# Optimization experiments

Hardware: AMD Instinct MI355X
Metric: run time of the kernel (lower is better)

The kernel has to match this reference:

```python
import jax, jax.numpy as jnp
import numpy as np

NU, NI, D, K, L, E, B = 500000, 200000, 64, 4, 3, 2000000, 131072

def setup_inputs() -> dict:
    key = jax.random.key(0)
    ks = jax.random.split(key, 7)
    return {
        'user_emb': 0.1 * jax.random.normal(ks[0], (NU, D), dtype=jnp.float32),
        'item_emb': 0.1 * jax.random.normal(ks[1], (NI, D), dtype=jnp.float32),
        'factor_weight': jax.random.normal(ks[2], (K, K), dtype=jnp.float32),
        'edge_users': jax.random.randint(ks[3], (E,), 0, NU),
        'edge_items': jax.random.randint(ks[4], (E,), 0, NI),
        'users': jax.random.randint(ks[5], (B,), 0, NU),
        'items': jax.random.randint(ks[6], (B,), 0, NI),
    }

def reference(user_emb, item_emb, factor_weight, edge_users, edge_items, users, items):
    N = NU + NI
    X = jnp.concatenate([user_emb, item_emb], axis=0)  # [N, D]
    src = edge_users                     # user node ids
    dst = edge_items + NU                # item node ids (offset)
    # symmetric degree normalization 1/sqrt(d_u * d_i) over the bipartite graph
    deg = jnp.zeros((N,), jnp.float32).at[src].add(1.0).at[dst].add(1.0)
    inv_sqrt = jnp.where(deg > 0, jax.lax.rsqrt(jnp.maximum(deg, 1.0)), 0.0)
    w = (inv_sqrt[src] * inv_sqrt[dst])[:, None]  # [E, 1]

    def propagate(x):
        # messages in both directions (A is symmetric)
        out = jnp.zeros_like(x)
        out = out.at[dst].add(x[src] * w)
        out = out.at[src].add(x[dst] * w)
        return out

    acc = X
    x = X
    for _ in range(L):
        x = propagate(x)
        acc = acc + x
    Z = acc / jnp.float32(L + 1)  # LightGCN layer mean

    dk = D // K
    u = Z[users].reshape(B, K, dk)          # user factor embeddings
    i = Z[items + NU].reshape(B, K, dk)     # item factor embeddings
    corr = jnp.einsum('bfd,bgd->bfg', u, i)  # pairwise factor correlations
    scores = jnp.einsum('bfg,fg->b', corr, factor_weight)
    return scores
```

## Files before the change

kernel.cpp:

```cpp
#include <hip/hip_runtime.h>
#include <math.h>

#define NU_ 500000
#define NI_ 200000
#define NN_ 700000
#define D_  64
#define E_  2000000
#define B_  131072
#define TWO_E 4000000

#define SHIFT_ 10
#define NBUCK_ 684
#define BCAP_  12288
#define B1_TILE 16384

typedef _Float16 half4 __attribute__((ext_vector_type(4)));
typedef _Float16 half8 __attribute__((ext_vector_type(8)));

__global__ __launch_bounds__(256) void bucket_hist_kernel(const int* __restrict__ eu,
                                                          const int* __restrict__ ei,
                                                          int* __restrict__ bucketCnt,
                                                          int* __restrict__ rowptr) {
    __shared__ int h[NBUCK_];
    for (int i = threadIdx.x; i < NBUCK_; i += 256) h[i] = 0;
    __syncthreads();
    size_t base = (size_t)blockIdx.x * B1_TILE;
    for (int k = 0; k < 64; ++k) {
        size_t idx = base + (size_t)k * 256 + threadIdx.x;
        if (idx < TWO_E) {
            int e = (int)(idx >> 1);
            int node = (idx & 1) ? (ei[e] + NU_) : eu[e];
            atomicAdd(&h[node >> SHIFT_], 1);
        }
    }
    __syncthreads();
    for (int i = threadIdx.x; i < NBUCK_; i += 256)
        if (h[i]) atomicAdd(&bucketCnt[i], h[i]);
    if (blockIdx.x == 0 && threadIdx.x == 0) rowptr[NN_] = TWO_E;
}

__global__ __launch_bounds__(1024) void scan_block(const int* __restrict__ in, int n,
                                                   int* __restrict__ out,
                                                   int* __restrict__ psum) {
    __shared__ int lds[1024];
    int g = blockIdx.x * 1024 + threadIdx.x;
    int v = (g < n) ? in[g] : 0;
    lds[threadIdx.x] = v;
    __syncthreads();
    for (int off = 1; off < 1024; off <<= 1) {
        int t = (threadIdx.x >= (unsigned)off) ? lds[threadIdx.x - off] : 0;
        __syncthreads();
        lds[threadIdx.x] += t;
        __syncthreads();
    }
    if (g < n) out[g] = lds[threadIdx.x] - v;
    if (threadIdx.x == 1023 && psum) psum[blockIdx.x] = lds[1023];
}

__global__ __launch_bounds__(256) void bucket_scatter_kernel(const int* __restrict__ eu,
                                                             const int* __restrict__ ei,
                                                             int* __restrict__ cursor,
                                                             unsigned long long* __restrict__ pairs) {
    __shared__ int h[NBUCK_];
    __shared__ int basel[NBUCK_];
    for (int i = threadIdx.x; i < NBUCK_; i += 256) h[i] = 0;
    __syncthreads();
    size_t base = (size_t)blockIdx.x * B1_TILE;
    for (int k = 0; k < 64; ++k) {
        size_t idx = base + (size_t)k * 256 + threadIdx.x;
        if (idx < TWO_E) {
            int e = (int)(idx >> 1);
            int node = (idx & 1) ? (ei[e] + NU_) : eu[e];
            atomicAdd(&h[node >> SHIFT_], 1);
        }
    }
    __syncthreads();
    for (int i = threadIdx.x; i < NBUCK_; i += 256) {
        int c = h[i];
        basel[i] = c ? atomicAdd(&cursor[i], c) : 0;
    }
    __syncthreads();
    for (int i = threadIdx.x; i < NBUCK_; i += 256) h[i] = 0;
    __syncthreads();
    for (int k = 0; k < 64; ++k) {
        size_t idx = base + (size_t)k * 256 + threadIdx.x;
        if (idx < TWO_E) {
            int e = (int)(idx >> 1);
            int side = (int)(idx & 1);
            int u = eu[e];
            int v = ei[e] + NU_;
            int node = side ? v : u;
            int nbr  = side ? u : v;
            int bk = node >> SHIFT_;
            int r = atomicAdd(&h[bk], 1);
            pairs[(size_t)basel[bk] + r] =
                ((unsigned long long)(unsigned)node << 32) | (unsigned)nbr;
        }
    }
}

__global__ __launch_bounds__(256) void csr_build_kernel(const unsigned long long* __restrict__ pairs,
                                                        const int* __restrict__ bucketBase,
                                                        int* __restrict__ rowptr,
                                                        int* __restrict__ adj,
                                                        float* __restrict__ inv,
                                                        float* __restrict__ sdeg) {
    __shared__ int cnt[1024];
    __shared__ int sA[1024];
    __shared__ int sB[1024];
    __shared__ int adjl[BCAP_];
    int b  = blockIdx.x;
    int lo = bucketBase[b];
    int hi = (b == NBUCK_ - 1) ? TWO_E : bucketBase[b + 1];
    int sz = hi - lo;
    if (sz > BCAP_) sz = BCAP_;
    int node0 = b << SHIFT_;
    for (int i = threadIdx.x; i < 1024; i += 256) cnt[i] = 0;
    __syncthreads();
    for (int i = threadIdx.x; i < sz; i += 256) {
        int node = (int)(pairs[(size_t)lo + i] >> 32);
        atomicAdd(&cnt[node & 1023], 1);
    }
    __syncthreads();
    for (int i = threadIdx.x; i < 1024; i += 256) sA[i] = cnt[i];
    __syncthreads();
    int* cur = sA; int* nxt = sB;
    for (int off = 1; off < 1024; off <<= 1) {
        for (int i = threadIdx.x; i < 1024; i += 256)
            nxt[i] = cur[i] + (i >= off ? cur[i - off] : 0);
        __syncthreads();
        int* tmp = cur; cur = nxt; nxt = tmp;
    }
    for (int i = threadIdx.x; i < 1024; i += 256) {
        int excl = cur[i] - cnt[i];
        nxt[i] = excl;
        int node = node0 + i;
        if (node < NN_) {
            rowptr[node] = lo + excl;
            int d = cnt[i];
            inv[node]  = d ? (1.0f / sqrtf((float)d)) : 0.0f;
            sdeg[node] = sqrtf((float)d);
        }
    }
    __syncthreads();
    for (int i = threadIdx.x; i < sz; i += 256) {
        unsigned long long p = pairs[(size_t)lo + i];
        int node = (int)(p >> 32);
        int nbr  = (int)(p & 0xffffffffu);
        int r = atomicAdd(&nxt[node & 1023], 1);
        if (r < BCAP_) adjl[r] = nbr;
    }
    __syncthreads();
    for (int i = threadIdx.x; i < sz; i += 256) adj[lo + i] = adjl[i];
}

__global__ __launch_bounds__(256) void conv_kernel(const float* __restrict__ ue,
                                                   const float* __restrict__ ie,
                                                   const float* __restrict__ inv,
                                                   half4* __restrict__ xh) {
    int t = blockIdx.x * 256 + threadIdx.x;
    int b = t >> 4;
    int q = t & 15;
    const float4* src = (b < NU_)
        ? ((const float4*)(ue + (size_t)b * D_) + q)
        : ((const float4*)(ie + (size_t)(b - NU_) * D_) + q);
    float4 a = *src;
    float iv = inv[b];
    half4 h;
    h[0] = (_Float16)(iv * a.x); h[1] = (_Float16)(iv * a.y);
    h[2] = (_Float16)(iv * a.z); h[3] = (_Float16)(iv * a.w);
    xh[(size_t)b * 16 + q] = h;
}

__global__ __launch_bounds__(256) void pull_kernel(const half8* __restrict__ yh,
                                                   const float* __restrict__ inv,
                                                   const int* __restrict__ rowptr,
                                                   const int* __restrict__ adj,
                                                   half8* __restrict__ out) {
    int t = blockIdx.x * 256 + threadIdx.x;
    int v = t >> 6;
    int lane = t & 63;
    int g = lane >> 3;
    int q = lane & 7;
    int beg = rowptr[v];
    int end = rowptr[v + 1];
    float acc[8] = {0.f, 0.f, 0.f, 0.f, 0.f, 0.f, 0.f, 0.f};
    for (int j = beg; j < end; j += 8) {
        int i = j + g;
        int n = adj[i];
        n = (i < end) ? n : NN_;
        half8 a = yh[(size_t)n * 8 + q];
#pragma unroll
        for (int k = 0; k < 8; ++k)
            acc[k] += (float)a[k];
    }
#pragma unroll
    for (int k = 0; k < 8; ++k) {
        acc[k] += __shfl_xor(acc[k], 8);
        acc[k] += __shfl_xor(acc[k], 16);
        acc[k] += __shfl_xor(acc[k], 32);
    }
    if (g == 0) {
        float iv = inv[v];
        float iv2 = iv * iv;
        half8 o;
#pragma unroll
        for (int k = 0; k < 8; ++k) o[k] = (_Float16)(iv2 * acc[k]);
        out[(size_t)v * 8 + q] = o;
    }
}

__device__ __forceinline__ float node_final(int node,
                                            const float* __restrict__ embrow,
                                            const _Float16* __restrict__ y1,
                                            const _Float16* __restrict__ y2,
                                            const float* __restrict__ inv,
                                            const float* __restrict__ sdeg,
                                            const int* __restrict__ rowptr,
                                            const int* __restrict__ adj,
                                            int lane, int g, int q) {
    int beg = rowptr[node];
    int end = rowptr[node + 1];
    float acc[8] = {0.f, 0.f, 0.f, 0.f, 0.f, 0.f, 0.f, 0.f};
    for (int j = beg; j < end; j += 8) {
        int i = j + g;
        int n = adj[i];
        n = (i < end) ? n : NN_;
        half8 a = *(const half8*)(y2 + ((unsigned)n * 64u + (unsigned)q * 8u));
#pragma unroll
        for (int k = 0; k < 8; ++k)
            acc[k] += (float)a[k];
    }
#pragma unroll
    for (int k = 0; k < 8; ++k) {
        acc[k] += __shfl_xor(acc[k], 8);
        acc[k] += __shfl_xor(acc[k], 16);
        acc[k] += __shfl_xor(acc[k], 32);
    }
    float red = 0.0f;
#pragma unroll
    for (int k = 0; k < 8; ++k) {
        float tmp = __shfl(acc[k], lane >> 3);
        red = ((lane & 7) == k) ? tmp : red;
    }
    float s   = sdeg[node];
    float l12 = ((float)y1[(unsigned)node * 64u + (unsigned)lane]
               + (float)y2[(unsigned)node * 64u + (unsigned)lane]) * s;
    return embrow[lane] + l12 + inv[node] * red;
}

__global__ __launch_bounds__(256) void final_score_kernel(
        const float* __restrict__ ue,
        const float* __restrict__ ie,
        const _Float16* __restrict__ y1,
        const _Float16* __restrict__ y2,
        const float* __restrict__ inv,
        const float* __restrict__ sdeg,
        const int* __restrict__ rowptr,
        const int* __restrict__ adj,
        const int* __restrict__ users,
        const int* __restrict__ items,
        const float* __restrict__ fw,
        float* __restrict__ out) {
    int t = blockIdx.x * 256 + threadIdx.x;
    int b = t >> 6;
    int lane = t & 63;
    int g = lane >> 3;
    int q = lane & 7;

    int u  = users[b];
    int io = items[b];
    int it = io + NU_;
    float zu = node_final(u,  ue + (size_t)u * D_,  y1, y2, inv, sdeg, rowptr, adj, lane, g, q);
    float zi = node_final(it, ie + (size_t)io * D_, y1, y2, inv, sdeg, rowptr, adj, lane, g, q);

    int f = lane >> 4;
    float s = 0.0f;
#pragma unroll
    for (int gg = 0; gg < 4; ++gg) {
        float pi = __shfl(zi, (gg << 4) | (lane & 15));
        float p = zu * pi;
        p += __shfl_xor(p, 1);
        p += __shfl_xor(p, 2);
        p += __shfl_xor(p, 4);
        p += __shfl_xor(p, 8);
        s += fw[f * 4 + gg] * p;
    }
    s += __shfl_xor(s, 16);
    s += __shfl_xor(s, 32);
    if (lane == 0) out[b] = s * 0.0625f;
}

extern "C" void kernel_launch(void* const* d_in, const int* in_sizes, int n_in,
                              void* d_out, int out_size, void* d_ws, size_t ws_size,
                              hipStream_t stream) {
    const float* ue    = (const float*)d_in[0];
    const float* ie    = (const float*)d_in[1];
    const float* fw    = (const float*)d_in[2];
    const int*   eu    = (const int*)d_in[3];
    const int*   eitem = (const int*)d_in[4];
    const int*   users = (const int*)d_in[5];
    const int*   items = (const int*)d_in[6];
    float* scores = (float*)d_out;

    const size_t xh_bytes = (size_t)(NN_ + 1) * D_ * 2;

    char* ws = (char*)d_ws;
    half8* X0h  = (half8*)ws;  ws += xh_bytes;
    half8* XAh  = (half8*)ws;  ws += xh_bytes;
    unsigned long long* pairs = (unsigned long long*)ws; ws += (size_t)TWO_E * 8;
    int*   adj  = (int*)ws;    ws += (size_t)TWO_E * 4;
    int*   rowptr = (int*)ws;  ws += (size_t)(NN_ + 1) * 4;
    float* inv  = (float*)ws;  ws += (size_t)NN_ * 4;
    float* sdeg = (float*)ws;  ws += (size_t)NN_ * 4;
    int*   bucketCnt  = (int*)ws; ws += (size_t)NBUCK_ * 4;
    int*   bucketBase = (int*)ws; ws += (size_t)NBUCK_ * 4;
    int*   cursor     = (int*)ws; ws += (size_t)NBUCK_ * 4;
    half8* XBh  = X0h;

    hipMemsetAsync(bucketCnt, 0, (size_t)NBUCK_ * 4, stream);
    hipMemsetAsync((char*)X0h + (size_t)NN_ * 128, 0, 128, stream);
    hipMemsetAsync((char*)XAh + (size_t)NN_ * 128, 0, 128, stream);
    const int NB1 = (TWO_E + B1_TILE - 1) / B1_TILE;
    bucket_hist_kernel<<<NB1, 256, 0, stream>>>(eu, eitem, bucketCnt, rowptr);
    scan_block<<<1, 1024, 0, stream>>>(bucketCnt, NBUCK_, bucketBase, (int*)nullptr);
    hipMemcpyAsync(cursor, bucketBase, (size_t)NBUCK_ * 4, hipMemcpyDeviceToDevice, stream);
    bucket_scatter_kernel<<<NB1, 256, 0, stream>>>(eu, eitem, cursor, pairs);
    csr_build_kernel<<<NBUCK_, 256, 0, stream>>>(pairs, bucketBase, rowptr, adj, inv, sdeg);

    conv_kernel<<<(NN_ * 16) / 256, 256, 0, stream>>>(ue, ie, inv, (half4*)X0h);

    pull_kernel<<<(NN_ * D_) / 256, 256, 0, stream>>>(X0h, inv, rowptr, adj, XAh);
    pull_kernel<<<(NN_ * D_) / 256, 256, 0, stream>>>(XAh, inv, rowptr, adj, XBh);

    final_score_kernel<<<(B_ * D_) / 256, 256, 0, stream>>>(
        ue, ie, (const _Float16*)XAh, (const _Float16*)XBh,
        inv, sdeg, rowptr, adj, users, items, fw, scores);
}
```

Before: 749.3 us.

## Use per-block bucket histograms, packed 32-bit pairs, and interleaved final gathers

The histogram pass now writes per-block, per-bucket counts that a multi-level scan turns into fixed scatter offsets. This lets the scatter kernel skip its second histogram pass and its global atomic cursor. Edge pairs are packed into 32 bits (10-bit local node, 20-bit neighbor), halving the pairs traffic, which relies on node ids fitting in 20 bits. The final score kernel interleaves the user and item neighbor gathers in one loop to expose more memory-level parallelism, at the cost of extra scan launches and more registers.

Result: faster. 716.8 us (-4.3%).

```diff
diff --git a/kernel.cpp b/kernel.cpp
--- a/kernel.cpp
+++ b/kernel.cpp
@@ -13,13 +13,16 @@
 #define NBUCK_ 684
 #define BCAP_  12288
 #define B1_TILE 16384
+#define NB1_   245
+#define NTOT_  (NBUCK_ * NB1_)
+#define NSCAN2_ ((NTOT_ + 1023) / 1024)
 
 typedef _Float16 half4 __attribute__((ext_vector_type(4)));
 typedef _Float16 half8 __attribute__((ext_vector_type(8)));
 
 __global__ __launch_bounds__(256) void bucket_hist_kernel(const int* __restrict__ eu,
                                                           const int* __restrict__ ei,
-                                                          int* __restrict__ bucketCnt,
+                                                          int* __restrict__ blockHist,
                                                           int* __restrict__ rowptr) {
     __shared__ int h[NBUCK_];
     for (int i = threadIdx.x; i < NBUCK_; i += 256) h[i] = 0;
@@ -35,7 +38,7 @@
     }
     __syncthreads();
     for (int i = threadIdx.x; i < NBUCK_; i += 256)
-        if (h[i]) atomicAdd(&bucketCnt[i], h[i]);
+        blockHist[(size_t)i * NB1_ + blockIdx.x] = h[i];
     if (blockIdx.x == 0 && threadIdx.x == 0) rowptr[NN_] = TWO_E;
 }
 
@@ -57,31 +60,25 @@
     if (threadIdx.x == 1023 && psum) psum[blockIdx.x] = lds[1023];
 }
 
+__global__ __launch_bounds__(256) void scan_add_kernel(int* __restrict__ a,
+                                                       const int* __restrict__ poff,
+                                                       int n) {
+    int g = blockIdx.x * 256 + threadIdx.x;
+    if (g < n) a[g] += poff[g >> 10];
+}
+
 __global__ __launch_bounds__(256) void bucket_scatter_kernel(const int* __restrict__ eu,
                                                              const int* __restrict__ ei,
-                                                             int* __restrict__ cursor,
-                                                             unsigned long long* __restrict__ pairs) {
+                                                             const int* __restrict__ bhScan,
+                                                             unsigned int* __restrict__ pairs) {
     __shared__ int h[NBUCK_];
     __shared__ int basel[NBUCK_];
-    for (int i = threadIdx.x; i < NBUCK_; i += 256) h[i] = 0;
+    for (int i = threadIdx.x; i < NBUCK_; i += 256) {
+        h[i] = 0;
+        basel[i] = bhScan[(size_t)i * NB1_ + blockIdx.x];
+    }
     __syncthreads();
     size_t base = (size_t)blockIdx.x * B1_TILE;
-    for (int k = 0; k < 64; ++k) {
-        size_t idx = base + (size_t)k * 256 + threadIdx.x;
-        if (idx < TWO_E) {
-            int e = (int)(idx >> 1);
-            int node = (idx & 1) ? (ei[e] + NU_) : eu[e];
-            atomicAdd(&h[node >> SHIFT_], 1);
-        }
-    }
-    __syncthreads();
-    for (int i = threadIdx.x; i < NBUCK_; i += 256) {
-        int c = h[i];
-        basel[i] = c ? atomicAdd(&cursor[i], c) : 0;
-    }
-    __syncthreads();
-    for (int i = threadIdx.x; i < NBUCK_; i += 256) h[i] = 0;
-    __syncthreads();
     for (int k = 0; k < 64; ++k) {
         size_t idx = base + (size_t)k * 256 + threadIdx.x;
         if (idx < TWO_E) {
@@ -94,13 +91,13 @@
             int bk = node >> SHIFT_;
             int r = atomicAdd(&h[bk], 1);
             pairs[(size_t)basel[bk] + r] =
-                ((unsigned long long)(unsigned)node << 32) | (unsigned)nbr;
+                ((unsigned)(node & 1023) << 20) | (unsigned)nbr;
         }
     }
 }
 
-__global__ __launch_bounds__(256) void csr_build_kernel(const unsigned long long* __restrict__ pairs,
-                                                        const int* __restrict__ bucketBase,
+__global__ __launch_bounds__(256) void csr_build_kernel(const unsigned int* __restrict__ pairs,
+                                                        const int* __restrict__ bhScan,
                                                         int* __restrict__ rowptr,
                                                         int* __restrict__ adj,
                                                         float* __restrict__ inv,
@@ -110,16 +107,15 @@
     __shared__ int sB[1024];
     __shared__ int adjl[BCAP_];
     int b  = blockIdx.x;
-    int lo = bucketBase[b];
-    int hi = (b == NBUCK_ - 1) ? TWO_E : bucketBase[b + 1];
+    int lo = bhScan[(size_t)b * NB1_];
+    int hi = (b == NBUCK_ - 1) ? TWO_E : bhScan[(size_t)(b + 1) * NB1_];
     int sz = hi - lo;
     if (sz > BCAP_) sz = BCAP_;
     int node0 = b << SHIFT_;
     for (int i = threadIdx.x; i < 1024; i += 256) cnt[i] = 0;
     __syncthreads();
     for (int i = threadIdx.x; i < sz; i += 256) {
-        int node = (int)(pairs[(size_t)lo + i] >> 32);
-        atomicAdd(&cnt[node & 1023], 1);
+        atomicAdd(&cnt[pairs[(size_t)lo + i] >> 20], 1);
     }
     __syncthreads();
     for (int i = threadIdx.x; i < 1024; i += 256) sA[i] = cnt[i];
@@ -144,11 +140,9 @@
     }
     __syncthreads();
     for (int i = threadIdx.x; i < sz; i += 256) {
-        unsigned long long p = pairs[(size_t)lo + i];
-        int node = (int)(p >> 32);
-        int nbr  = (int)(p & 0xffffffffu);
-        int r = atomicAdd(&nxt[node & 1023], 1);
-        if (r < BCAP_) adjl[r] = nbr;
+        unsigned int p = pairs[(size_t)lo + i];
+        int r = atomicAdd(&nxt[p >> 20], 1);
+        if (r < BCAP_) adjl[r] = (int)(p & 0xFFFFFu);
     }
     __syncthreads();
     for (int i = threadIdx.x; i < sz; i += 256) adj[lo + i] = adjl[i];
@@ -210,45 +204,6 @@
     }
 }
 
-__device__ __forceinline__ float node_final(int node,
-                                            const float* __restrict__ embrow,
-                                            const _Float16* __restrict__ y1,
-                                            const _Float16* __restrict__ y2,
-                                            const float* __restrict__ inv,
-                                            const float* __restrict__ sdeg,
-                                            const int* __restrict__ rowptr,
-                                            const int* __restrict__ adj,
-                                            int lane, int g, int q) {
-    int beg = rowptr[node];
-    int end = rowptr[node + 1];
-    float acc[8] = {0.f, 0.f, 0.f, 0.f, 0.f, 0.f, 0.f, 0.f};
-    for (int j = beg; j < end; j += 8) {
-        int i = j + g;
-        int n = adj[i];
-        n = (i < end) ? n : NN_;
-        half8 a = *(const half8*)(y2 + ((unsigned)n * 64u + (unsigned)q * 8u));
-#pragma unroll
-        for (int k = 0; k < 8; ++k)
-            acc[k] += (float)a[k];
-    }
-#pragma unroll
-    for (int k = 0; k < 8; ++k) {
-        acc[k] += __shfl_xor(acc[k], 8);
-        acc[k] += __shfl_xor(acc[k], 16);
-        acc[k] += __shfl_xor(acc[k], 32);
-    }
-    float red = 0.0f;
-#pragma unroll
-    for (int k = 0; k < 8; ++k) {
-        float tmp = __shfl(acc[k], lane >> 3);
-        red = ((lane & 7) == k) ? tmp : red;
-    }
-    float s   = sdeg[node];
-    float l12 = ((float)y1[(unsigned)node * 64u + (unsigned)lane]
-               + (float)y2[(unsigned)node * 64u + (unsigned)lane]) * s;
-    return embrow[lane] + l12 + inv[node] * red;
-}
-
 __global__ __launch_bounds__(256) void final_score_kernel(
         const float* __restrict__ ue,
         const float* __restrict__ ie,
@@ -271,8 +226,53 @@
     int u  = users[b];
     int io = items[b];
     int it = io + NU_;
-    float zu = node_final(u,  ue + (size_t)u * D_,  y1, y2, inv, sdeg, rowptr, adj, lane, g, q);
-    float zi = node_final(it, ie + (size_t)io * D_, y1, y2, inv, sdeg, rowptr, adj, lane, g, q);
+    int begU = rowptr[u],  endU = rowptr[u + 1];
+    int begI = rowptr[it], endI = rowptr[it + 1];
+    int nsU = (endU - begU + 7) >> 3;
+    int nsI = (endI - begI + 7) >> 3;
+    int steps = nsU > nsI ? nsU : nsI;
+
+    float aU[8] = {0.f,0.f,0.f,0.f,0.f,0.f,0.f,0.f};
+    float aI[8] = {0.f,0.f,0.f,0.f,0.f,0.f,0.f,0.f};
+    for (int s = 0; s < steps; ++s) {
+        int iu = begU + 8 * s + g;
+        int ii = begI + 8 * s + g;
+        int nU = adj[iu];
+        int nI = adj[ii];
+        nU = (iu < endU) ? nU : NN_;
+        nI = (ii < endI) ? nI : NN_;
+        half8 au = *(const half8*)(y2 + ((unsigned)nU * 64u + (unsigned)q * 8u));
+        half8 ai = *(const half8*)(y2 + ((unsigned)nI * 64u + (unsigned)q * 8u));
+#pragma unroll
+        for (int k = 0; k < 8; ++k) {
+            aU[k] += (float)au[k];
+            aI[k] += (float)ai[k];
+        }
+    }
+#pragma unroll
+    for (int k = 0; k < 8; ++k) {
+        aU[k] += __shfl_xor(aU[k], 8);
+        aI[k] += __shfl_xor(aI[k], 8);
+        aU[k] += __shfl_xor(aU[k], 16);
+        aI[k] += __shfl_xor(aI[k], 16);
+        aU[k] += __shfl_xor(aU[k], 32);
+        aI[k] += __shfl_xor(aI[k], 32);
+    }
+    float redU = 0.0f, redI = 0.0f;
+#pragma unroll
+    for (int k = 0; k < 8; ++k) {
+        float tU = __shfl(aU[k], lane >> 3);
+        float tI = __shfl(aI[k], lane >> 3);
+        if ((lane & 7) == k) { redU = tU; redI = tI; }
+    }
+    float zu = ue[(size_t)u * D_ + lane]
+             + ((float)y1[(unsigned)u * 64u + (unsigned)lane]
+              + (float)y2[(unsigned)u * 64u + (unsigned)lane]) * sdeg[u]
+             + inv[u] * redU;
+    float zi = ie[(size_t)io * D_ + lane]
+             + ((float)y1[(unsigned)it * 64u + (unsigned)lane]
+              + (float)y2[(unsigned)it * 64u + (unsigned)lane]) * sdeg[it]
+             + inv[it] * redI;
 
     int f = lane >> 4;
     float s = 0.0f;
@@ -308,25 +308,25 @@
     char* ws = (char*)d_ws;
     half8* X0h  = (half8*)ws;  ws += xh_bytes;
     half8* XAh  = (half8*)ws;  ws += xh_bytes;
-    unsigned long long* pairs = (unsigned long long*)ws; ws += (size_t)TWO_E * 8;
+    unsigned int* pairs = (unsigned int*)ws; ws += (size_t)TWO_E * 4;
     int*   adj  = (int*)ws;    ws += (size_t)TWO_E * 4;
     int*   rowptr = (int*)ws;  ws += (size_t)(NN_ + 1) * 4;
     float* inv  = (float*)ws;  ws += (size_t)NN_ * 4;
     float* sdeg = (float*)ws;  ws += (size_t)NN_ * 4;
-    int*   bucketCnt  = (int*)ws; ws += (size_t)NBUCK_ * 4;
-    int*   bucketBase = (int*)ws; ws += (size_t)NBUCK_ * 4;
-    int*   cursor     = (int*)ws; ws += (size_t)NBUCK_ * 4;
+    int*   blockHist = (int*)ws; ws += (size_t)NTOT_ * 4;
+    int*   bhScan    = (int*)ws; ws += (size_t)NTOT_ * 4;
+    int*   psum2     = (int*)ws; ws += (size_t)NSCAN2_ * 4;
+    int*   poff2     = (int*)ws; ws += (size_t)NSCAN2_ * 4;
     half8* XBh  = X0h;
 
-    hipMemsetAsync(bucketCnt, 0, (size_t)NBUCK_ * 4, stream);
     hipMemsetAsync((char*)X0h + (size_t)NN_ * 128, 0, 128, stream);
     hipMemsetAsync((char*)XAh + (size_t)NN_ * 128, 0, 128, stream);
-    const int NB1 = (TWO_E + B1_TILE - 1) / B1_TILE;
-    bucket_hist_kernel<<<NB1, 256, 0, stream>>>(eu, eitem, bucketCnt, rowptr);
-    scan_block<<<1, 1024, 0, stream>>>(bucketCnt, NBUCK_, bucketBase, (int*)nullptr);
-    hipMemcpyAsync(cursor, bucketBase, (size_t)NBUCK_ * 4, hipMemcpyDeviceToDevice, stream);
-    bucket_scatter_kernel<<<NB1, 256, 0, stream>>>(eu, eitem, cursor, pairs);
-    csr_build_kernel<<<NBUCK_, 256, 0, stream>>>(pairs, bucketBase, rowptr, adj, inv, sdeg);
+    bucket_hist_kernel<<<NB1_, 256, 0, stream>>>(eu, eitem, blockHist, rowptr);
+    scan_block<<<NSCAN2_, 1024, 0, stream>>>(blockHist, NTOT_, bhScan, psum2);
+    scan_block<<<1, 1024, 0, stream>>>(psum2, NSCAN2_, poff2, (int*)nullptr);
+    scan_add_kernel<<<(NTOT_ + 255) / 256, 256, 0, stream>>>(bhScan, poff2, NTOT_);
+    bucket_scatter_kernel<<<NB1_, 256, 0, stream>>>(eu, eitem, bhScan, pairs);
+    csr_build_kernel<<<NBUCK_, 256, 0, stream>>>(pairs, bhScan, rowptr, adj, inv, sdeg);
 
     conv_kernel<<<(NN_ * 16) / 256, 256, 0, stream>>>(ue, ie, inv, (half4*)X0h);
 
```
